# Kernel tuning notes

Measured on AMD Instinct MI355X. Metric: run time of the kernel, lower is better.

The kernel has to match this reference:

```python
import jax, jax.numpy as jnp
import numpy as np

B, L, D, H = 1, 4096, 1024, 16
HD = D // H  # head dim = 64
WINDOW = 15


def _rope(t, cos, sin):
    # t: [B,H,L,HD]; cos/sin: [1,1,L,HD//2]
    tr = t.reshape(*t.shape[:-1], HD // 2, 2)
    a, b = tr[..., 0], tr[..., 1]
    out_r = a * cos - b * sin
    out_i = a * sin + b * cos
    return jnp.stack([out_r, out_i], axis=-1).reshape(t.shape)


def _longformer_mask(L, window):
    i = jnp.arange(L)[:, None]
    j = jnp.arange(L)[None, :]
    causal = j <= i
    win = jnp.abs(i - j) <= window // 2
    glob = (j == 0) | (i == 0)
    return (causal & win) | glob  # [L,L] bool


def setup_inputs() -> dict:
    key = jax.random.key(0)
    kx, kq, kk, kv, ko = jax.random.split(key, 5)
    x = jax.random.normal(kx, (B, L, D), dtype=jnp.float32)
    scale = 0.02
    Wq = jax.random.normal(kq, (D, D), dtype=jnp.float32) * scale
    Wk = jax.random.normal(kk, (D, D), dtype=jnp.float32) * scale
    Wv = jax.random.normal(kv, (D, D), dtype=jnp.float32) * scale
    Wo = jax.random.normal(ko, (D, D), dtype=jnp.float32) * scale
    # real RoPE frequencies (complex freqs_cis split into cos/sin)
    inv_freq = 1.0 / (10000.0 ** (np.arange(0, HD, 2, dtype=np.float32) / HD))
    pos = np.arange(L, dtype=np.float32)
    ang = pos[:, None] * inv_freq[None, :]  # [L, HD//2]
    freqs_cos = jnp.asarray(np.cos(ang))[None]  # [1,L,HD//2]
    freqs_sin = jnp.asarray(np.sin(ang))[None]
    return {"x": x, "Wq": Wq, "Wk": Wk, "Wv": Wv, "Wo": Wo,
            "freqs_cos": freqs_cos, "freqs_sin": freqs_sin}


def reference(x, Wq, Wk, Wv, Wo, freqs_cos, freqs_sin):
    b, l, _ = x.shape
    # projections (nn.Linear: y = x @ W^T)
    Q = (x @ Wq.T).reshape(b, l, H, HD).transpose(0, 2, 1, 3)  # [B,H,L,HD]
    K = (x @ Wk.T).reshape(b, l, H, HD).transpose(0, 2, 1, 3)
    V = (x @ Wv.T).reshape(b, l, H, HD).transpose(0, 2, 1, 3)
    cos = freqs_cos[:, None, :l]  # [1,1,L,HD//2] (torch unsqueeze(1))
    sin = freqs_sin[:, None, :l]
    Q = _rope(Q, cos, sin)
    K = _rope(K, cos, sin)
    mask = _longformer_mask(l, WINDOW)  # [L,L]
    scores = jnp.einsum('bhqd,bhkd->bhqk', Q, K) / jnp.sqrt(jnp.float32(HD))
    scores = jnp.where(mask[None, None], scores, jnp.finfo(scores.dtype).min)
    attn = jax.nn.softmax(scores, axis=-1)
    out = jnp.einsum('bhqk,bhkd->bhqd', attn, V)  # [B,H,L,HD]
    out = out.transpose(0, 2, 1, 3).reshape(b, l, D)
    return out @ Wo.T
```

## Files before the change

kernel.cpp:

```cpp
#include <hip/hip_runtime.h>
#include <stdint.h>

#define SL 4096
#define DM 1024
#define NH 16
#define HDIM 64

typedef short short8 __attribute__((ext_vector_type(8)));
typedef float f32x4 __attribute__((ext_vector_type(4)));

__device__ __forceinline__ unsigned short f2bf(float f) {
  unsigned int u = __float_as_uint(f);
  u += 0x7FFF + ((u >> 16) & 1);
  return (unsigned short)(u >> 16);
}
__device__ __forceinline__ float bf2f(unsigned short u) {
  return __uint_as_float((unsigned int)u << 16);
}
__device__ __forceinline__ float bflo(unsigned int u) { return __uint_as_float(u << 16); }
__device__ __forceinline__ float bfhi(unsigned int u) { return __uint_as_float(u & 0xffff0000u); }

__device__ __forceinline__ void gload_lds16(const void* g, void* l) {
  __builtin_amdgcn_global_load_lds((const __attribute__((address_space(1))) void*)g,
                                   (__attribute__((address_space(3))) void*)l, 16, 0, 0);
}
#define SBAR()                                  \
  do {                                          \
    __builtin_amdgcn_sched_barrier(0);          \
    __builtin_amdgcn_s_barrier();               \
    __builtin_amdgcn_sched_barrier(0);          \
  } while (0)

__global__ void cast_all(const float* __restrict__ x,
                         const float* __restrict__ Wq, const float* __restrict__ Wk,
                         const float* __restrict__ Wv, const float* __restrict__ Wo,
                         unsigned short* __restrict__ xb,
                         unsigned short* __restrict__ w3b, unsigned short* __restrict__ wob) {
  int i = blockIdx.x * blockDim.x + threadIdx.x;
  const float* src;
  unsigned short* dst;
  int off;
  if (i < (1 << 20)) {
    src = x; dst = xb; off = i;
  } else {
    int wsel = i - (1 << 20);
    int seg = wsel >> 18;
    off = wsel & 262143;
    src = (seg == 0) ? Wq : (seg == 1) ? Wk : (seg == 2) ? Wv : Wo;
    dst = (seg < 3) ? (w3b + (size_t)seg * DM * DM) : wob;
  }
  float4 v = ((const float4*)src)[off];
  ushort4 o = make_ushort4(f2bf(v.x), f2bf(v.y), f2bf(v.z), f2bf(v.w));
  ((ushort4*)dst)[off] = o;
}

__global__ __launch_bounds__(512)
void gemm256_rope(const unsigned short* __restrict__ A,
                  const unsigned short* __restrict__ B,
                  unsigned short* __restrict__ C,
                  const float* __restrict__ fc, const float* __restrict__ fs) {
  constexpr int K = 1024, LDA = 1024, LDC = 3072, NT = K / 64;
  __shared__ __align__(16) unsigned short As[2][256 * 64];
  __shared__ __align__(16) unsigned short Bs[2][256 * 64];
  const int tid = threadIdx.x, w = tid >> 6, lane = tid & 63;
  const int wr = w >> 2, wc = w & 3;

  const int gx = gridDim.x;
  const int total = gx * gridDim.y;
  const int lin = blockIdx.y * gx + blockIdx.x;
  const int swz = (lin & 7) * (total >> 3) + (lin >> 3);
  const int brow = (swz / gx) * 256;
  const int bcol = (swz % gx) * 256;

  const unsigned short* gA[2];
  const unsigned short* gB[2];
#pragma unroll
  for (int l = 0; l < 2; ++l) {
    int idx = l * 512 + tid;
    int row_l = idx >> 3, c = idx & 7;
    int csrc = c ^ ((row_l >> 1) & 7);
    gA[l] = A + (size_t)(brow + row_l) * LDA + csrc * 8;
    gB[l] = B + (size_t)(bcol + row_l) * LDA + csrc * 8;
  }

  auto STG_A = [&](int t, int h) {
    const int buf = t & 1;
#pragma unroll
    for (int l = 0; l < 2; ++l)
      gload_lds16(gA[l] + (size_t)h * 128 * LDA + t * 64,
                  &As[buf][h * 8192 + (l * 512 + w * 64) * 8]);
  };
  auto STG_B = [&](int t, int h) {
    const int buf = t & 1;
#pragma unroll
    for (int l = 0; l < 2; ++l)
      gload_lds16(gB[l] + (size_t)h * 128 * LDA + t * 64,
                  &Bs[buf][h * 8192 + (l * 512 + w * 64) * 8]);
  };

  const int lrow = lane & 15, h4 = lane >> 4;
  const int g3 = (lane >> 1) & 7;
  const int u2 = h4 ^ (g3 & 3);
  const int gv = g3 >> 2;
  const int co0 = ((((0 ^ gv) << 2) | u2)) * 8;
  const int co1 = ((((1 ^ gv) << 2) | u2)) * 8;

  f32x4 acc[8][4] = {};
  short8 a0[8], a1[8], b0[4], b1[4];

  STG_A(0, 0); STG_A(0, 1); STG_B(0, 0); STG_B(0, 1); STG_A(1, 0); STG_A(1, 1);
  asm volatile("s_waitcnt vmcnt(4)" ::: "memory");
  SBAR();

  for (int t = 0; t < NT; ++t) {
    const int buf = t & 1;
    const unsigned short* Ab = &As[buf][(wr * 128 + lrow) * 64];
    const unsigned short* Bb = &Bs[buf][(wc * 64 + lrow) * 64];
#pragma unroll
    for (int n = 0; n < 4; ++n) b0[n] = *(const short8*)&Bb[n * 16 * 64 + co0];
#pragma unroll
    for (int m = 0; m < 8; ++m) a0[m] = *(const short8*)&Ab[m * 16 * 64 + co0];
    if (t + 1 < NT) STG_B(t + 1, 0);
    SBAR();
    __builtin_amdgcn_s_setprio(1);
#pragma unroll
    for (int m = 0; m < 8; ++m) {
      acc[m][0] = __builtin_amdgcn_mfma_f32_16x16x32_bf16(a0[m], b0[0], acc[m][0], 0, 0, 0);
      acc[m][1] = __builtin_amdgcn_mfma_f32_16x16x32_bf16(a0[m], b0[1], acc[m][1], 0, 0, 0);
    }
    __builtin_amdgcn_s_setprio(0);
#pragma unroll
    for (int n = 0; n < 4; ++n) b1[n] = *(const short8*)&Bb[n * 16 * 64 + co1];
#pragma unroll
    for (int m = 0; m < 8; ++m) a1[m] = *(const short8*)&Ab[m * 16 * 64 + co1];
    if (t + 1 < NT) STG_B(t + 1, 1);
    SBAR();
    __builtin_amdgcn_s_setprio(1);
#pragma unroll
    for (int m = 0; m < 8; ++m) {
      acc[m][2] = __builtin_amdgcn_mfma_f32_16x16x32_bf16(a0[m], b0[2], acc[m][2], 0, 0, 0);
      acc[m][3] = __builtin_amdgcn_mfma_f32_16x16x32_bf16(a0[m], b0[3], acc[m][3], 0, 0, 0);
    }
    __builtin_amdgcn_s_setprio(0);
    if (t + 2 < NT) STG_A(t + 2, 0);
    SBAR();
    __builtin_amdgcn_s_setprio(1);
#pragma unroll
    for (int m = 0; m < 8; ++m) {
      acc[m][0] = __builtin_amdgcn_mfma_f32_16x16x32_bf16(a1[m], b1[0], acc[m][0], 0, 0, 0);
      acc[m][1] = __builtin_amdgcn_mfma_f32_16x16x32_bf16(a1[m], b1[1], acc[m][1], 0, 0, 0);
    }
    __builtin_amdgcn_s_setprio(0);
    if (t + 2 < NT) STG_A(t + 2, 1);
    if (t >= NT - 2) {
      asm volatile("s_waitcnt vmcnt(0)" ::: "memory");
    } else {
      asm volatile("s_waitcnt vmcnt(4)" ::: "memory");
    }
    SBAR();
    __builtin_amdgcn_s_setprio(1);
#pragma unroll
    for (int m = 0; m < 8; ++m) {
      acc[m][2] = __builtin_amdgcn_mfma_f32_16x16x32_bf16(a1[m], b1[2], acc[m][2], 0, 0, 0);
      acc[m][3] = __builtin_amdgcn_mfma_f32_16x16x32_bf16(a1[m], b1[3], acc[m][3], 0, 0, 0);
    }
    __builtin_amdgcn_s_setprio(0);
  }

  const int er = (lane >> 4) * 4;
  const int ec = lane & 15;
  if (bcol + wc * 64 < 2048) {
#pragma unroll
    for (int n = 0; n < 4; ++n) {
      const int p = ((n * 16 + ec) & 63) >> 1;
#pragma unroll
      for (int m = 0; m < 8; ++m) {
#pragma unroll
        for (int r = 0; r < 4; ++r) {
          const int row = brow + wr * 128 + m * 16 + er + r;
          float v = acc[m][n][r];
          float pv = __shfl_xor(v, 1);
          float cs = fc[row * 32 + p], sn = fs[row * 32 + p];
          acc[m][n][r] = (lane & 1) ? (pv * sn + v * cs) : (v * cs - pv * sn);
        }
      }
    }
  }
#pragma unroll
  for (int m = 0; m < 8; ++m)
#pragma unroll
    for (int n = 0; n < 4; ++n) {
      unsigned short* cp = C + (size_t)(brow + wr * 128 + m * 16 + er) * LDC +
                           (bcol + wc * 64 + n * 16 + ec);
#pragma unroll
      for (int r = 0; r < 4; ++r) cp[(size_t)r * LDC] = f2bf(acc[m][n][r]);
    }
}

template <int BM, int BN, bool BF16OUT, bool ROPE>
__global__ void gemm_bt(const unsigned short* __restrict__ A,
                        const unsigned short* __restrict__ B,
                        void* __restrict__ Cv,
                        int K, int lda, int ldc, size_t czstride,
                        const float* __restrict__ fc, const float* __restrict__ fs) {
  constexpr int WM = BM / 64, WN = BN / 64, W = WM * WN;
  constexpr int ACW = BM / 16 / W;
  constexpr int BCW = BN / 16 / W;
  __shared__ __align__(16) unsigned short As[2][BM * 32];
  __shared__ __align__(16) unsigned short Bs[2][BN * 32];
  const int tid  = threadIdx.x;
  const int w    = tid >> 6;
  const int lane = tid & 63;
  const int wr = w / WN, wc = w % WN;

  const int kz = blockIdx.z;
  A += (size_t)kz * K;
  B += (size_t)kz * K;

  const int gx = gridDim.x;
  const int total = gx * gridDim.y;
  const int lin = blockIdx.y * gx + blockIdx.x;
  const int swz = (lin & 7) * (total >> 3) + (lin >> 3);
  const int brow = (swz / gx) * BM;
  const int bcol = (swz % gx) * BN;

  const int l4 = lane >> 2;
  const int lkS = (((lane & 3) ^ ((lane >> 3) & 3))) * 8;
  const int lrow = lane & 15;
  const int sw8 = (((lane >> 4) ^ ((lane >> 1) & 3))) * 8;

  const unsigned short* Ag[ACW];
  const unsigned short* Bg[BCW];
#pragma unroll
  for (int c = 0; c < ACW; ++c)
    Ag[c] = A + (size_t)(brow + (w * ACW + c) * 16 + l4) * lda + lkS;
#pragma unroll
  for (int c = 0; c < BCW; ++c)
    Bg[c] = B + (size_t)(bcol + (w * BCW + c) * 16 + l4) * lda + lkS;

  f32x4 acc[4][4] = {};
  const int NT = K >> 5;

  auto STAGE = [&](int t, int b) {
    const int k0 = t << 5;
#pragma unroll
    for (int c = 0; c < ACW; ++c) gload_lds16(Ag[c] + k0, &As[b][(w * ACW + c) * 512]);
#pragma unroll
    for (int c = 0; c < BCW; ++c) gload_lds16(Bg[c] + k0, &Bs[b][(w * BCW + c) * 512]);
  };
  auto COMPUTE = [&](int cur) {
    short8 af[4], bf[4];
#pragma unroll
    for (int m = 0; m < 4; ++m)
      af[m] = *(const short8*)&As[cur][(wr * 64 + m * 16 + lrow) * 32 + sw8];
#pragma unroll
    for (int n = 0; n < 4; ++n)
      bf[n] = *(const short8*)&Bs[cur][(wc * 64 + n * 16 + lrow) * 32 + sw8];
#pragma unroll
    for (int m = 0; m < 4; ++m)
#pragma unroll
      for (int n = 0; n < 4; ++n)
        acc[m][n] = __builtin_amdgcn_mfma_f32_16x16x32_bf16(af[m], bf[n], acc[m][n], 0, 0, 0);
  };

  STAGE(0, 0);
  for (int t = 0; t < NT; ++t) {
    const int cur = t & 1;
    __syncthreads();
    if (t + 1 < NT) STAGE(t + 1, cur ^ 1);
    COMPUTE(cur);
  }

  const int er = (lane >> 4) * 4;
  const int ec = lane & 15;

  if constexpr (ROPE) {
    if (bcol + wc * 64 < 2048) {
#pragma unroll
      for (int n = 0; n < 4; ++n) {
        const int p = ((n * 16 + ec) & 63) >> 1;
#pragma unroll
        for (int m = 0; m < 4; ++m) {
#pragma unroll
          for (int r = 0; r < 4; ++r) {
            const int row = brow + wr * 64 + m * 16 + er + r;
            float v = acc[m][n][r];
            float pv = __shfl_xor(v, 1);
            float cs = fc[row * 32 + p], sn = fs[row * 32 + p];
            acc[m][n][r] = (lane & 1) ? (pv * sn + v * cs) : (v * cs - pv * sn);
          }
        }
      }
    }
  }

#pragma unroll
  for (int m = 0; m < 4; ++m)
#pragma unroll
    for (int n = 0; n < 4; ++n) {
      const size_t roff = (size_t)(brow + wr * 64 + m * 16 + er) * ldc + (bcol + wc * 64 + n * 16 + ec);
      if constexpr (BF16OUT) {
        unsigned short* cp = (unsigned short*)Cv + roff;
#pragma unroll
        for (int r = 0; r < 4; ++r) cp[(size_t)r * ldc] = f2bf(acc[m][n][r]);
      } else {
        float* cp = (float*)Cv + kz * czstride + roff;
#pragma unroll
        for (int r = 0; r < 4; ++r) cp[(size_t)r * ldc] = acc[m][n][r];
      }
    }
}

__global__ __launch_bounds__(256)
void attn_fused(const unsigned short* __restrict__ qkv, unsigned short* __restrict__ atb,
                float* __restrict__ prt) {
  const int wid = threadIdx.x >> 6;
  const int lane = threadIdx.x & 63;
  if (blockIdx.x >= 1024) {
    const int u = (blockIdx.x - 1024) * 4 + wid;
    const int p = u & 127, h = u >> 7;
    const float q = bf2f(qkv[h * 64 + lane]);
    float m = -1e30f, s = 0.f, o = 0.f;
    const int j0 = p * 32;
    for (int jj = 0; jj < 32; ++jj) {
      const int j = j0 + jj;
      float kv = bf2f(qkv[(size_t)j * 3072 + 1024 + h * 64 + lane]);
      float pr = q * kv;
#pragma unroll
      for (int off = 32; off; off >>= 1) pr += __shfl_xor(pr, off);
      pr *= 0.125f;
      float mn = fmaxf(m, pr);
      float c = __expf(m - mn);
      float e = __expf(pr - mn);
      float v = bf2f(qkv[(size_t)j * 3072 + 2048 + h * 64 + lane]);
      s = s * c + e;
      o = o * c + e * v;
      m = mn;
    }
    float* dst = prt + ((size_t)h * 128 + p) * 72;
    if (lane == 0) { dst[0] = m; dst[1] = s; }
    dst[2 + lane] = o;
    return;
  }

  const int i = blockIdx.x * 4 + wid + 1;
  if (i >= SL) return;
  const unsigned short* rowQ = qkv + (size_t)i * 3072 + lane * 16;

  float q[16];
  {
    uint4 a = *(const uint4*)rowQ;
    uint4 b = *(const uint4*)(rowQ + 8);
    unsigned int uu[8] = {a.x, a.y, a.z, a.w, b.x, b.y, b.z, b.w};
#pragma unroll
    for (int c = 0; c < 8; ++c) { q[2 * c] = bflo(uu[c]); q[2 * c + 1] = bfhi(uu[c]); }
  }

  float sc[9];
#pragma unroll
  for (int t = 0; t < 9; ++t) {
    int j = (t == 0) ? 0 : (i - 8 + t);
    bool valid = (t == 0) || (j >= 1);
    int jc = valid ? j : 0;
    const unsigned short* pk = qkv + (size_t)jc * 3072 + 1024 + lane * 16;
    uint4 a = *(const uint4*)pk;
    uint4 b = *(const uint4*)(pk + 8);
    unsigned int uu[8] = {a.x, a.y, a.z, a.w, b.x, b.y, b.z, b.w};
    float pr = 0.f;
#pragma unroll
    for (int c = 0; c < 8; ++c) pr += bflo(uu[c]) * q[2 * c] + bfhi(uu[c]) * q[2 * c + 1];
    pr += __shfl_xor(pr, 1);
    pr += __shfl_xor(pr, 2);
    sc[t] = valid ? pr * 0.125f : -1e30f;
  }

  float mx = sc[0];
#pragma unroll
  for (int t = 1; t < 9; ++t) mx = fmaxf(mx, sc[t]);
  float s = 0.f;
#pragma unroll
  for (int t = 0; t < 9; ++t) { float e = __expf(sc[t] - mx); sc[t] = e; s += e; }
  const float inv = 1.0f / s;

  float o[16] = {};
#pragma unroll
  for (int t = 0; t < 9; ++t) {
    int j = (t == 0) ? 0 : (i - 8 + t);
    bool valid = (t == 0) || (j >= 1);
    int jc = valid ? j : 0;
    const unsigned short* pv = qkv + (size_t)jc * 3072 + 2048 + lane * 16;
    uint4 a = *(const uint4*)pv;
    uint4 b = *(const uint4*)(pv + 8);
    unsigned int uu[8] = {a.x, a.y, a.z, a.w, b.x, b.y, b.z, b.w};
#pragma unroll
    for (int c = 0; c < 8; ++c) {
      o[2 * c]     += sc[t] * bflo(uu[c]);
      o[2 * c + 1] += sc[t] * bfhi(uu[c]);
    }
  }

  unsigned int wv[8];
#pragma unroll
  for (int c = 0; c < 8; ++c)
    wv[c] = (unsigned int)f2bf(o[2 * c] * inv) | ((unsigned int)f2bf(o[2 * c + 1] * inv) << 16);
  unsigned short* po = atb + (size_t)i * 1024 + lane * 16;
  uint4 s0; s0.x = wv[0]; s0.y = wv[1]; s0.z = wv[2]; s0.w = wv[3];
  uint4 s1; s1.x = wv[4]; s1.y = wv[5]; s1.z = wv[6]; s1.w = wv[7];
  *(uint4*)po = s0;
  *(uint4*)(po + 8) = s1;
}

__global__ __launch_bounds__(64)
void attn_row0_combine(const float* __restrict__ prt, unsigned short* __restrict__ atb) {
  const int h = blockIdx.x;
  const int lane = threadIdx.x;
  const float* base = prt + (size_t)h * 128 * 72;
  __shared__ float cbuf[128];
  float m0 = base[lane * 72];
  float m1 = base[(lane + 64) * 72];
  float M = fmaxf(m0, m1);
#pragma unroll
  for (int off = 32; off; off >>= 1) M = fmaxf(M, __shfl_xor(M, off));
  float c0 = __expf(m0 - M), c1 = __expf(m1 - M);
  float ls = base[lane * 72 + 1] * c0 + base[(lane + 64) * 72 + 1] * c1;
#pragma unroll
  for (int off = 32; off; off >>= 1) ls += __shfl_xor(ls, off);
  cbuf[lane] = c0;
  cbuf[lane + 64] = c1;
  __syncthreads();
  float o = 0.f;
#pragma unroll 8
  for (int p = 0; p < 128; ++p) o += cbuf[p] * base[p * 72 + 2 + lane];
  atb[h * 64 + lane] = f2bf(o / ls);
}

extern "C" void kernel_launch(void* const* d_in, const int* in_sizes, int n_in,
                              void* d_out, int out_size, void* d_ws, size_t ws_size,
                              hipStream_t stream) {
  const float* x  = (const float*)d_in[0];
  const float* Wq = (const float*)d_in[1];
  const float* Wk = (const float*)d_in[2];
  const float* Wv = (const float*)d_in[3];
  const float* Wo = (const float*)d_in[4];
  const float* fc = (const float*)d_in[5];
  const float* fs = (const float*)d_in[6];
  float* out = (float*)d_out;

  char* ws = (char*)d_ws;
  unsigned short* xb   = (unsigned short*)(ws);
  unsigned short* w3b  = (unsigned short*)(ws + ((size_t)8 << 20));
  unsigned short* wob  = (unsigned short*)(ws + ((size_t)14 << 20));
  unsigned short* qkvb = (unsigned short*)(ws + ((size_t)16 << 20));
  unsigned short* atb  = (unsigned short*)(ws + ((size_t)40 << 20));
  float*          prt  = (float*)(ws + ((size_t)48 << 20));

  cast_all<<<(2 * (1 << 20)) / 256, 256, 0, stream>>>(x, Wq, Wk, Wv, Wo, xb, w3b, wob);

  dim3 g1(3072 / 256, SL / 256);
  gemm256_rope<<<g1, 512, 0, stream>>>(xb, w3b, qkvb, fc, fs);

  attn_fused<<<1536, 256, 0, stream>>>(qkvb, atb, prt);
  attn_row0_combine<<<NH, 64, 0, stream>>>(prt, atb);

  dim3 g2(DM / 128, SL / 128, 1);
  gemm_bt<128, 128, false, false><<<g2, 256, 0, stream>>>(
      atb, wob, (void*)out, DM, DM, DM, 0, nullptr, nullptr);
}
```

Baseline: 98.11 us.

## Retile QKV GEMM to 256x192 and port output GEMM to 4-phase pipeline

The QKV projection GEMM changes its block tile from 256x256 to 256x192. That gives 16x16=256 blocks, matching the 256 CUs of the chip and avoiding a partial second wave. The RoPE epilogue is adjusted per 16-column subtile, since a warp's 48 columns can now straddle the Q/K/V boundaries. The output projection GEMM drops the generic 32-wide-K double-buffered kernel for a specialized 64-wide-K kernel with the same interleaved load/MFMA phase schedule and setprio used by the first GEMM. Both kernels add an explicit LDS wait before a barrier, and the new tile shape gives an uneven phase split for B loads.

```diff
diff --git a/kernel.cpp b/kernel.cpp
--- a/kernel.cpp
+++ b/kernel.cpp
@@ -30,6 +30,7 @@
     __builtin_amdgcn_s_barrier();               \
     __builtin_amdgcn_sched_barrier(0);          \
   } while (0)
+#define LGKM0() asm volatile("s_waitcnt lgkmcnt(0)" ::: "memory")
 
 __global__ void cast_all(const float* __restrict__ x,
                          const float* __restrict__ Wq, const float* __restrict__ Wk,
@@ -55,13 +56,13 @@
 }
 
 __global__ __launch_bounds__(512)
-void gemm256_rope(const unsigned short* __restrict__ A,
-                  const unsigned short* __restrict__ B,
-                  unsigned short* __restrict__ C,
-                  const float* __restrict__ fc, const float* __restrict__ fs) {
+void gemm1_rope(const unsigned short* __restrict__ A,
+                const unsigned short* __restrict__ B,
+                unsigned short* __restrict__ C,
+                const float* __restrict__ fc, const float* __restrict__ fs) {
   constexpr int K = 1024, LDA = 1024, LDC = 3072, NT = K / 64;
   __shared__ __align__(16) unsigned short As[2][256 * 64];
-  __shared__ __align__(16) unsigned short Bs[2][256 * 64];
+  __shared__ __align__(16) unsigned short Bs[2][192 * 64];
   const int tid = threadIdx.x, w = tid >> 6, lane = tid & 63;
   const int wr = w >> 2, wc = w & 3;
 
@@ -70,16 +71,22 @@
   const int lin = blockIdx.y * gx + blockIdx.x;
   const int swz = (lin & 7) * (total >> 3) + (lin >> 3);
   const int brow = (swz / gx) * 256;
-  const int bcol = (swz % gx) * 256;
+  const int bcol = (swz % gx) * 192;
 
   const unsigned short* gA[2];
-  const unsigned short* gB[2];
+  const unsigned short* gB[3];
 #pragma unroll
   for (int l = 0; l < 2; ++l) {
     int idx = l * 512 + tid;
     int row_l = idx >> 3, c = idx & 7;
     int csrc = c ^ ((row_l >> 1) & 7);
     gA[l] = A + (size_t)(brow + row_l) * LDA + csrc * 8;
+  }
+#pragma unroll
+  for (int l = 0; l < 3; ++l) {
+    int idx = l * 512 + tid;
+    int row_l = idx >> 3, c = idx & 7;
+    int csrc = c ^ ((row_l >> 1) & 7);
     gB[l] = B + (size_t)(bcol + row_l) * LDA + csrc * 8;
   }
 
@@ -90,12 +97,15 @@
       gload_lds16(gA[l] + (size_t)h * 128 * LDA + t * 64,
                   &As[buf][h * 8192 + (l * 512 + w * 64) * 8]);
   };
-  auto STG_B = [&](int t, int h) {
+  auto STG_B_a = [&](int t) {
     const int buf = t & 1;
 #pragma unroll
     for (int l = 0; l < 2; ++l)
-      gload_lds16(gB[l] + (size_t)h * 128 * LDA + t * 64,
-                  &Bs[buf][h * 8192 + (l * 512 + w * 64) * 8]);
+      gload_lds16(gB[l] + t * 64, &Bs[buf][(l * 512 + w * 64) * 8]);
+  };
+  auto STG_B_b = [&](int t) {
+    const int buf = t & 1;
+    gload_lds16(gB[2] + t * 64, &Bs[buf][(2 * 512 + w * 64) * 8]);
   };
 
   const int lrow = lane & 15, h4 = lane >> 4;
@@ -105,22 +115,22 @@
   const int co0 = ((((0 ^ gv) << 2) | u2)) * 8;
   const int co1 = ((((1 ^ gv) << 2) | u2)) * 8;
 
-  f32x4 acc[8][4] = {};
-  short8 a0[8], a1[8], b0[4], b1[4];
-
-  STG_A(0, 0); STG_A(0, 1); STG_B(0, 0); STG_B(0, 1); STG_A(1, 0); STG_A(1, 1);
+  f32x4 acc[8][3] = {};
+  short8 a0[8], a1[8], b0[3], b1[3];
+
+  STG_A(0, 0); STG_A(0, 1); STG_B_a(0); STG_B_b(0); STG_A(1, 0); STG_A(1, 1);
   asm volatile("s_waitcnt vmcnt(4)" ::: "memory");
   SBAR();
 
   for (int t = 0; t < NT; ++t) {
     const int buf = t & 1;
     const unsigned short* Ab = &As[buf][(wr * 128 + lrow) * 64];
-    const unsigned short* Bb = &Bs[buf][(wc * 64 + lrow) * 64];
-#pragma unroll
-    for (int n = 0; n < 4; ++n) b0[n] = *(const short8*)&Bb[n * 16 * 64 + co0];
+    const unsigned short* Bb = &Bs[buf][(wc * 48 + lrow) * 64];
+#pragma unroll
+    for (int n = 0; n < 3; ++n) b0[n] = *(const short8*)&Bb[n * 16 * 64 + co0];
 #pragma unroll
     for (int m = 0; m < 8; ++m) a0[m] = *(const short8*)&Ab[m * 16 * 64 + co0];
-    if (t + 1 < NT) STG_B(t + 1, 0);
+    if (t + 1 < NT) STG_B_a(t + 1);
     SBAR();
     __builtin_amdgcn_s_setprio(1);
 #pragma unroll
@@ -130,17 +140,16 @@
     }
     __builtin_amdgcn_s_setprio(0);
 #pragma unroll
-    for (int n = 0; n < 4; ++n) b1[n] = *(const short8*)&Bb[n * 16 * 64 + co1];
+    for (int n = 0; n < 3; ++n) b1[n] = *(const short8*)&Bb[n * 16 * 64 + co1];
 #pragma unroll
     for (int m = 0; m < 8; ++m) a1[m] = *(const short8*)&Ab[m * 16 * 64 + co1];
-    if (t + 1 < NT) STG_B(t + 1, 1);
-    SBAR();
-    __builtin_amdgcn_s_setprio(1);
-#pragma unroll
-    for (int m = 0; m < 8; ++m) {
+    if (t + 1 < NT) STG_B_b(t + 1);
+    LGKM0();
+    SBAR();
+    __builtin_amdgcn_s_setprio(1);
+#pragma unroll
+    for (int m = 0; m < 8; ++m)
       acc[m][2] = __builtin_amdgcn_mfma_f32_16x16x32_bf16(a0[m], b0[2], acc[m][2], 0, 0, 0);
-      acc[m][3] = __builtin_amdgcn_mfma_f32_16x16x32_bf16(a0[m], b0[3], acc[m][3], 0, 0, 0);
-    }
     __builtin_amdgcn_s_setprio(0);
     if (t + 2 < NT) STG_A(t + 2, 0);
     SBAR();
@@ -160,19 +169,17 @@
     SBAR();
     __builtin_amdgcn_s_setprio(1);
 #pragma unroll
-    for (int m = 0; m < 8; ++m) {
+    for (int m = 0; m < 8; ++m)
       acc[m][2] = __builtin_amdgcn_mfma_f32_16x16x32_bf16(a1[m], b1[2], acc[m][2], 0, 0, 0);
-      acc[m][3] = __builtin_amdgcn_mfma_f32_16x16x32_bf16(a1[m], b1[3], acc[m][3], 0, 0, 0);
-    }
     __builtin_amdgcn_s_setprio(0);
   }
 
   const int er = (lane >> 4) * 4;
   const int ec = lane & 15;
-  if (bcol + wc * 64 < 2048) {
-#pragma unroll
-    for (int n = 0; n < 4; ++n) {
-      const int p = ((n * 16 + ec) & 63) >> 1;
+#pragma unroll
+  for (int n = 0; n < 3; ++n) {
+    if (bcol + wc * 48 + n * 16 < 2048) {
+      const int p = ((wc * 48 + n * 16 + ec) & 63) >> 1;
 #pragma unroll
       for (int m = 0; m < 8; ++m) {
 #pragma unroll
@@ -189,125 +196,135 @@
 #pragma unroll
   for (int m = 0; m < 8; ++m)
 #pragma unroll
-    for (int n = 0; n < 4; ++n) {
+    for (int n = 0; n < 3; ++n) {
       unsigned short* cp = C + (size_t)(brow + wr * 128 + m * 16 + er) * LDC +
-                           (bcol + wc * 64 + n * 16 + ec);
+                           (bcol + wc * 48 + n * 16 + ec);
 #pragma unroll
       for (int r = 0; r < 4; ++r) cp[(size_t)r * LDC] = f2bf(acc[m][n][r]);
     }
 }
 
-template <int BM, int BN, bool BF16OUT, bool ROPE>
-__global__ void gemm_bt(const unsigned short* __restrict__ A,
-                        const unsigned short* __restrict__ B,
-                        void* __restrict__ Cv,
-                        int K, int lda, int ldc, size_t czstride,
-                        const float* __restrict__ fc, const float* __restrict__ fs) {
-  constexpr int WM = BM / 64, WN = BN / 64, W = WM * WN;
-  constexpr int ACW = BM / 16 / W;
-  constexpr int BCW = BN / 16 / W;
-  __shared__ __align__(16) unsigned short As[2][BM * 32];
-  __shared__ __align__(16) unsigned short Bs[2][BN * 32];
-  const int tid  = threadIdx.x;
-  const int w    = tid >> 6;
-  const int lane = tid & 63;
-  const int wr = w / WN, wc = w % WN;
-
-  const int kz = blockIdx.z;
-  A += (size_t)kz * K;
-  B += (size_t)kz * K;
+__global__ __launch_bounds__(256)
+void gemm2_4ph(const unsigned short* __restrict__ A,
+               const unsigned short* __restrict__ B,
+               float* __restrict__ C) {
+  constexpr int K = 1024, LDA = 1024, LDC = 1024, NT = K / 64;
+  __shared__ __align__(16) unsigned short As2[2][128 * 64];
+  __shared__ __align__(16) unsigned short Bs2[2][128 * 64];
+  const int tid = threadIdx.x, w = tid >> 6, lane = tid & 63;
+  const int wr = w >> 1, wc = w & 1;
 
   const int gx = gridDim.x;
   const int total = gx * gridDim.y;
   const int lin = blockIdx.y * gx + blockIdx.x;
   const int swz = (lin & 7) * (total >> 3) + (lin >> 3);
-  const int brow = (swz / gx) * BM;
-  const int bcol = (swz % gx) * BN;
-
-  const int l4 = lane >> 2;
-  const int lkS = (((lane & 3) ^ ((lane >> 3) & 3))) * 8;
-  const int lrow = lane & 15;
-  const int sw8 = (((lane >> 4) ^ ((lane >> 1) & 3))) * 8;
-
-  const unsigned short* Ag[ACW];
-  const unsigned short* Bg[BCW];
-#pragma unroll
-  for (int c = 0; c < ACW; ++c)
-    Ag[c] = A + (size_t)(brow + (w * ACW + c) * 16 + l4) * lda + lkS;
-#pragma unroll
-  for (int c = 0; c < BCW; ++c)
-    Bg[c] = B + (size_t)(bcol + (w * BCW + c) * 16 + l4) * lda + lkS;
+  const int brow = (swz / gx) * 128;
+  const int bcol = (swz % gx) * 128;
+
+  const unsigned short* gA[4];
+  const unsigned short* gB[4];
+#pragma unroll
+  for (int l = 0; l < 4; ++l) {
+    int idx = l * 256 + tid;
+    int row_l = idx >> 3, c = idx & 7;
+    int csrc = c ^ ((row_l >> 1) & 7);
+    gA[l] = A + (size_t)(brow + row_l) * LDA + csrc * 8;
+    gB[l] = B + (size_t)(bcol + row_l) * LDA + csrc * 8;
+  }
+
+  auto STG_A = [&](int t, int h) {
+    const int buf = t & 1;
+#pragma unroll
+    for (int l = 2 * h; l < 2 * h + 2; ++l)
+      gload_lds16(gA[l] + t * 64, &As2[buf][(l * 256 + w * 64) * 8]);
+  };
+  auto STG_B = [&](int t, int h) {
+    const int buf = t & 1;
+#pragma unroll
+    for (int l = 2 * h; l < 2 * h + 2; ++l)
+      gload_lds16(gB[l] + t * 64, &Bs2[buf][(l * 256 + w * 64) * 8]);
+  };
+
+  const int lrow = lane & 15, h4 = lane >> 4;
+  const int g3 = (lane >> 1) & 7;
+  const int u2 = h4 ^ (g3 & 3);
+  const int gv = g3 >> 2;
+  const int co0 = ((((0 ^ gv) << 2) | u2)) * 8;
+  const int co1 = ((((1 ^ gv) << 2) | u2)) * 8;
 
   f32x4 acc[4][4] = {};
-  const int NT = K >> 5;
-
-  auto STAGE = [&](int t, int b) {
-    const int k0 = t << 5;
-#pragma unroll
-    for (int c = 0; c < ACW; ++c) gload_lds16(Ag[c] + k0, &As[b][(w * ACW + c) * 512]);
-#pragma unroll
-    for (int c = 0; c < BCW; ++c) gload_lds16(Bg[c] + k0, &Bs[b][(w * BCW + c) * 512]);
-  };
-  auto COMPUTE = [&](int cur) {
-    short8 af[4], bf[4];
-#pragma unroll
-    for (int m = 0; m < 4; ++m)
-      af[m] = *(const short8*)&As[cur][(wr * 64 + m * 16 + lrow) * 32 + sw8];
-#pragma unroll
-    for (int n = 0; n < 4; ++n)
-      bf[n] = *(const short8*)&Bs[cur][(wc * 64 + n * 16 + lrow) * 32 + sw8];
-#pragma unroll
-    for (int m = 0; m < 4; ++m)
-#pragma unroll
-      for (int n = 0; n < 4; ++n)
-        acc[m][n] = __builtin_amdgcn_mfma_f32_16x16x32_bf16(af[m], bf[n], acc[m][n], 0, 0, 0);
-  };
-
-  STAGE(0, 0);
+  short8 a0[4], a1[4], b0[4], b1[4];
+
+  STG_A(0, 0); STG_A(0, 1); STG_B(0, 0); STG_B(0, 1); STG_A(1, 0); STG_A(1, 1);
+  asm volatile("s_waitcnt vmcnt(4)" ::: "memory");
+  SBAR();
+
   for (int t = 0; t < NT; ++t) {
-    const int cur = t & 1;
-    __syncthreads();
-    if (t + 1 < NT) STAGE(t + 1, cur ^ 1);
-    COMPUTE(cur);
+    const int buf = t & 1;
+    const unsigned short* Ab = &As2[buf][(wr * 64 + lrow) * 64];
+    const unsigned short* Bb = &Bs2[buf][(wc * 64 + lrow) * 64];
+#pragma unroll
+    for (int n = 0; n < 4; ++n) b0[n] = *(const short8*)&Bb[n * 16 * 64 + co0];
+#pragma unroll
+    for (int m = 0; m < 4; ++m) a0[m] = *(const short8*)&Ab[m * 16 * 64 + co0];
+    if (t + 1 < NT) STG_B(t + 1, 0);
+    SBAR();
+    __builtin_amdgcn_s_setprio(1);
+#pragma unroll
+    for (int m = 0; m < 4; ++m) {
+      acc[m][0] = __builtin_amdgcn_mfma_f32_16x16x32_bf16(a0[m], b0[0], acc[m][0], 0, 0, 0);
+      acc[m][1] = __builtin_amdgcn_mfma_f32_16x16x32_bf16(a0[m], b0[1], acc[m][1], 0, 0, 0);
+    }
+    __builtin_amdgcn_s_setprio(0);
+#pragma unroll
+    for (int n = 0; n < 4; ++n) b1[n] = *(const short8*)&Bb[n * 16 * 64 + co1];
+#pragma unroll
+    for (int m = 0; m < 4; ++m) a1[m] = *(const short8*)&Ab[m * 16 * 64 + co1];
+    if (t + 1 < NT) STG_B(t + 1, 1);
+    LGKM0();
+    SBAR();
+    __builtin_amdgcn_s_setprio(1);
+#pragma unroll
+    for (int m = 0; m < 4; ++m) {
+      acc[m][2] = __builtin_amdgcn_mfma_f32_16x16x32_bf16(a0[m], b0[2], acc[m][2], 0, 0, 0);
+      acc[m][3] = __builtin_amdgcn_mfma_f32_16x16x32_bf16(a0[m], b0[3], acc[m][3], 0, 0, 0);
+    }
+    __builtin_amdgcn_s_setprio(0);
+    if (t + 2 < NT) STG_A(t + 2, 0);
+    SBAR();
+    __builtin_amdgcn_s_setprio(1);
+#pragma unroll
+    for (int m = 0; m < 4; ++m) {
+      acc[m][0] = __builtin_amdgcn_mfma_f32_16x16x32_bf16(a1[m], b1[0], acc[m][0], 0, 0, 0);
+      acc[m][1] = __builtin_amdgcn_mfma_f32_16x16x32_bf16(a1[m], b1[1], acc[m][1], 0, 0, 0);
+    }
+    __builtin_amdgcn_s_setprio(0);
+    if (t + 2 < NT) STG_A(t + 2, 1);
+    if (t >= NT - 2) {
+      asm volatile("s_waitcnt vmcnt(0)" ::: "memory");
+    } else {
+      asm volatile("s_waitcnt vmcnt(4)" ::: "memory");
+    }
+    SBAR();
+    __builtin_amdgcn_s_setprio(1);
+#pragma unroll
+    for (int m = 0; m < 4; ++m) {
+      acc[m][2] = __builtin_amdgcn_mfma_f32_16x16x32_bf16(a1[m], b1[2], acc[m][2], 0, 0, 0);
+      acc[m][3] = __builtin_amdgcn_mfma_f32_16x16x32_bf16(a1[m], b1[3], acc[m][3], 0, 0, 0);
+    }
+    __builtin_amdgcn_s_setprio(0);
   }
 
   const int er = (lane >> 4) * 4;
   const int ec = lane & 15;
-
-  if constexpr (ROPE) {
-    if (bcol + wc * 64 < 2048) {
-#pragma unroll
-      for (int n = 0; n < 4; ++n) {
-        const int p = ((n * 16 + ec) & 63) >> 1;
-#pragma unroll
-        for (int m = 0; m < 4; ++m) {
-#pragma unroll
-          for (int r = 0; r < 4; ++r) {
-            const int row = brow + wr * 64 + m * 16 + er + r;
-            float v = acc[m][n][r];
-            float pv = __shfl_xor(v, 1);
-            float cs = fc[row * 32 + p], sn = fs[row * 32 + p];
-            acc[m][n][r] = (lane & 1) ? (pv * sn + v * cs) : (v * cs - pv * sn);
-          }
-        }
-      }
-    }
-  }
-
 #pragma unroll
   for (int m = 0; m < 4; ++m)
 #pragma unroll
     for (int n = 0; n < 4; ++n) {
-      const size_t roff = (size_t)(brow + wr * 64 + m * 16 + er) * ldc + (bcol + wc * 64 + n * 16 + ec);
-      if constexpr (BF16OUT) {
-        unsigned short* cp = (unsigned short*)Cv + roff;
-#pragma unroll
-        for (int r = 0; r < 4; ++r) cp[(size_t)r * ldc] = f2bf(acc[m][n][r]);
-      } else {
-        float* cp = (float*)Cv + kz * czstride + roff;
-#pragma unroll
-        for (int r = 0; r < 4; ++r) cp[(size_t)r * ldc] = acc[m][n][r];
-      }
+      float* cp = C + (size_t)(brow + wr * 64 + m * 16 + er) * LDC +
+                  (bcol + wc * 64 + n * 16 + ec);
+#pragma unroll
+      for (int r = 0; r < 4; ++r) cp[(size_t)r * LDC] = acc[m][n][r];
     }
 }
 
@@ -456,13 +473,12 @@
 
   cast_all<<<(2 * (1 << 20)) / 256, 256, 0, stream>>>(x, Wq, Wk, Wv, Wo, xb, w3b, wob);
 
-  dim3 g1(3072 / 256, SL / 256);
-  gemm256_rope<<<g1, 512, 0, stream>>>(xb, w3b, qkvb, fc, fs);
+  dim3 g1(3072 / 192, SL / 256);
+  gemm1_rope<<<g1, 512, 0, stream>>>(xb, w3b, qkvb, fc, fs);
 
   attn_fused<<<1536, 256, 0, stream>>>(qkvb, atb, prt);
   attn_row0_combine<<<NH, 64, 0, stream>>>(prt, atb);
 
-  dim3 g2(DM / 128, SL / 128, 1);
-  gemm_bt<128, 128, false, false><<<g2, 256, 0, stream>>>(
-      atb, wob, (void*)out, DM, DM, DM, 0, nullptr, nullptr);
-}
+  dim3 g2(DM / 128, SL / 128);
+  gemm2_4ph<<<g2, 256, 0, stream>>>(atb, wob, out);
+}
```

After: 92.25 us. -6.0%, faster.
